# Kernel tuning notes

Measured on AMD Instinct MI355X. Metric: run time of the kernel, lower is better.

## Reference

```python
import jax, jax.numpy as jnp
import numpy as np

B, L, D = 2, 2048, 1024
NUM_HEADS = 16
HEAD_DIM = D // NUM_HEADS


def setup_inputs() -> dict:
    key = jax.random.key(0)
    k1, k2 = jax.random.split(key)
    x = jax.random.normal(k1, (B, L, D), dtype=jnp.float32)
    # torch Linear(input_dim, 3*output_dim, bias=False); store as [in, 3*out] for x @ W
    W_qkv = jax.random.normal(k2, (D, 3 * D), dtype=jnp.float32) * (1.0 / np.sqrt(D))
    return {"x": x, "W_qkv": W_qkv}


def reference(x, W_qkv):
    b, l, d = x.shape
    h, hd = NUM_HEADS, HEAD_DIM
    qkv = x @ W_qkv                                  # [B, L, 3*D]
    qkv = qkv.reshape(b, l, 3, h, hd)
    q = jnp.transpose(qkv[:, :, 0], (0, 2, 1, 3))    # [B, H, L, hd]
    k = jnp.transpose(qkv[:, :, 1], (0, 2, 1, 3))
    v = jnp.transpose(qkv[:, :, 2], (0, 2, 1, 3))
    scale = 1.0 / jnp.sqrt(jnp.asarray(hd, dtype=x.dtype))
    scores = jnp.einsum('bhqd,bhkd->bhqk', q, k) * scale   # [B, H, L, L]
    causal = jnp.triu(jnp.ones((l, l), dtype=bool), k=1)   # True above diagonal -> masked
    scores = jnp.where(causal, -jnp.inf, scores)
    attn = jax.nn.softmax(scores, axis=-1)
    # dropout p=0.0 -> identity (eval mode)
    out = jnp.einsum('bhqk,bhkd->bhqd', attn, v)            # [B, H, L, hd]
    out = jnp.transpose(out, (0, 2, 1, 3)).reshape(b, l, h * hd)
    return out
```

## Files before the change

kernel.cpp:

```cpp
#include <hip/hip_runtime.h>
#include <hip/hip_bf16.h>
#include <math.h>

#define NB_L 2048
#define GM 4096
#define GN 3072
#define GK 1024
#define NROWS 65536
#define SCALE_L2E 0.180336880f

typedef float  f4v __attribute__((ext_vector_type(4)));
typedef short  s4v __attribute__((ext_vector_type(4)));
typedef short  s8v __attribute__((ext_vector_type(8)));

#define MFMA_16x16x32(a, b, c) __builtin_amdgcn_mfma_f32_16x16x32_bf16((a), (b), (c), 0, 0, 0)
#define MFMA_16x16x16(a, b, c) __builtin_amdgcn_mfma_f32_16x16x16bf16_1k((a), (b), (c), 0, 0, 0)

static __device__ __forceinline__ unsigned int bfpk(float a, float b) {
    __hip_bfloat162 h = __float22bfloat162_rn(float2{a, b});
    union { __hip_bfloat162 h2; unsigned int u; } cv; cv.h2 = h; return cv.u;
}
static __device__ __forceinline__ unsigned short bf1(float a) {
    union { __hip_bfloat16 h; unsigned short u; } cv; cv.h = __float2bfloat16(a); return cv.u;
}
static __device__ __forceinline__ float bf2f(unsigned short u) {
    union { unsigned int u; float f; } cv; cv.u = ((unsigned int)u) << 16; return cv.f;
}

static __device__ __forceinline__ void gl_lds16(const ushort* g, ushort* l) {
    __builtin_amdgcn_global_load_lds((const __attribute__((address_space(1))) void*)g,
                                     (__attribute__((address_space(3))) void*)l, 16, 0, 0);
}

__global__ __launch_bounds__(256) void conv_x(const float* __restrict__ X, ushort* __restrict__ Xb) {
    const int i = blockIdx.x * 256 + threadIdx.x;
    const float4 f0 = ((const float4*)X)[2 * i];
    const float4 f1 = ((const float4*)X)[2 * i + 1];
    uint4 u;
    u.x = bfpk(f0.x, f0.y); u.y = bfpk(f0.z, f0.w);
    u.z = bfpk(f1.x, f1.y); u.w = bfpk(f1.z, f1.w);
    ((uint4*)Xb)[i] = u;
}

__global__ __launch_bounds__(256) void conv_wt(const float* __restrict__ W, ushort* __restrict__ Wt) {
    __shared__ __align__(16) ushort T[64][72];
    const int t = threadIdx.x;
    const int k0 = blockIdx.x * 64, n0 = blockIdx.y * 64;
    {
        const int kr = t >> 2, nc0 = (t & 3) * 16;
        const float* src = W + (size_t)(k0 + kr) * GN + n0 + nc0;
#pragma unroll
        for (int u = 0; u < 4; ++u) {
            const float4 v = *(const float4*)(src + 4 * u);
            T[nc0 + 4 * u + 0][kr] = bf1(v.x);
            T[nc0 + 4 * u + 1][kr] = bf1(v.y);
            T[nc0 + 4 * u + 2][kr] = bf1(v.z);
            T[nc0 + 4 * u + 3][kr] = bf1(v.w);
        }
    }
    __syncthreads();
    {
        const int nr = t >> 2, kc0 = (t & 3) * 16;
        ushort* dst = Wt + (size_t)(n0 + nr) * GK + k0 + kc0;
        *(s8v*)dst       = *(const s8v*)&T[nr][kc0];
        *(s8v*)(dst + 8) = *(const s8v*)&T[nr][kc0 + 8];
    }
}

__global__ __launch_bounds__(256) void qkv_gemm_bf16(
    const ushort* __restrict__ Xb, const ushort* __restrict__ Wt,
    ushort* __restrict__ Qh, ushort* __restrict__ Kh, ushort* __restrict__ VT)
{
    __shared__ __align__(16) ushort As[2][4][128][8];
    __shared__ __align__(16) ushort Bs[2][4][128][8];
    const int tid = threadIdx.x;
    const int row0 = blockIdx.y * 128, col0 = blockIdx.x * 128;
    const int mA = tid & 127, k2a = tid >> 7;
    const int lane = tid & 63, w = tid >> 6;
    const int wr = w >> 1, wc = w & 1, lq = lane & 15, quad = lane >> 4;

    f4v acc[4][4];
#pragma unroll
    for (int g = 0; g < 4; ++g)
#pragma unroll
        for (int j = 0; j < 4; ++j) acc[g][j] = 0.f;

    const ushort* gA = Xb + (size_t)(row0 + mA) * GK + k2a * 8;
    const ushort* gB = Wt + (size_t)(col0 + mA) * GK + k2a * 8;

    gl_lds16(gA,      &As[0][k2a][mA][0]);
    gl_lds16(gA + 16, &As[0][k2a + 2][mA][0]);
    gl_lds16(gB,      &Bs[0][k2a][mA][0]);
    gl_lds16(gB + 16, &Bs[0][k2a + 2][mA][0]);

    for (int it = 0; it < 32; ++it) {
        const int cur = it & 1, nxt = cur ^ 1;
        __syncthreads();
        if (it + 1 < 32) {
            const int k0 = (it + 1) * 32;
            gl_lds16(gA + k0,      &As[nxt][k2a][mA][0]);
            gl_lds16(gA + k0 + 16, &As[nxt][k2a + 2][mA][0]);
            gl_lds16(gB + k0,      &Bs[nxt][k2a][mA][0]);
            gl_lds16(gB + k0 + 16, &Bs[nxt][k2a + 2][mA][0]);
        }
        s8v af[4], bfr[4];
#pragma unroll
        for (int g = 0; g < 4; ++g) af[g]  = *(const s8v*)&As[cur][quad][wr * 64 + g * 16 + lq][0];
#pragma unroll
        for (int j = 0; j < 4; ++j) bfr[j] = *(const s8v*)&Bs[cur][quad][wc * 64 + j * 16 + lq][0];
#pragma unroll
        for (int g = 0; g < 4; ++g)
#pragma unroll
            for (int j = 0; j < 4; ++j)
                acc[g][j] = MFMA_16x16x32(af[g], bfr[j], acc[g][j]);
    }

    const int part = blockIdx.x >> 3;
#pragma unroll
    for (int g = 0; g < 4; ++g)
#pragma unroll
        for (int j = 0; j < 4; ++j) {
            const int col = (col0 & 1023) + wc * 64 + j * 16 + lq;
            const int hh = col >> 6, d = col & 63;
#pragma unroll
            for (int r = 0; r < 4; ++r) {
                const int row = row0 + wr * 64 + g * 16 + quad * 4 + r;
                const int b = row >> 11, tok = row & 2047;
                const int bh = b * 16 + hh;
                if (part == 0) {
                    Qh[((size_t)bh * 2048 + tok) * 64 + d] = bf1(acc[g][j][r] * SCALE_L2E);
                } else if (part == 1) {
                    Kh[((size_t)bh * 2048 + tok) * 64 + (d ^ ((tok & 7) << 3))] = bf1(acc[g][j][r]);
                } else {
                    VT[((size_t)bh * 64 + d) * 2048 + (tok ^ ((d & 7) << 3))] = bf1(acc[g][j][r]);
                }
            }
        }
}

__global__ __launch_bounds__(256, 4) void attn_bf16(
    const ushort* __restrict__ Qh, const ushort* __restrict__ Kh,
    const ushort* __restrict__ VT, ushort* __restrict__ Opart, float* __restrict__ Lp)
{
    __shared__ __align__(16) ushort Ks[2][64 * 64];
    __shared__ __align__(16) ushort Vt[2][64 * 64];

    const int x = blockIdx.x;
    const int bh = x & 31;
    const int qlow = (x >> 5) & 7;
    const int s = (x >> 8) & 1;
    const int x9 = (x >> 9) & 1;
    const int qt = x9 ? (15 - qlow) : qlow;

    const int tid = threadIdx.x;
    const int w = tid >> 6, lane = tid & 63;
    const int lq = lane & 15, quad = lane >> 4;
    const int kswz = (lq & 7) << 3;
    const int qrow_base = qt * 128 + w * 32;
    const int diag = 2 * qt + (w >> 1);

    s8v qf[2][2];
#pragma unroll
    for (int qg = 0; qg < 2; ++qg)
#pragma unroll
        for (int sb = 0; sb < 2; ++sb)
            qf[qg][sb] = *(const s8v*)(Qh + ((size_t)bh * 2048 + qrow_base + qg * 16 + lq) * 64
                                       + sb * 32 + quad * 8);

    f4v o[4][2];
#pragma unroll
    for (int dg = 0; dg < 4; ++dg)
#pragma unroll
        for (int qg = 0; qg < 2; ++qg) o[dg][qg] = 0.f;
    f4v lacc[2]; lacc[0] = 0.f; lacc[1] = 0.f;
    const s4v ones = { (short)0x3F80, (short)0x3F80, (short)0x3F80, (short)0x3F80 };

    const int kt_lo = s ? (qt + 1) : 0;
    const int kt_hi = s ? (2 * qt + 1) : qt;
    const int niter = kt_hi - kt_lo + 1;

    const ushort* kbase = Kh + (size_t)bh * 2048 * 64;
    const ushort* vbase = VT + (size_t)bh * 64 * 2048;
    const int g1 = tid, g2 = tid + 256;
    const int kr1 = g1 >> 3, ko1 = (g1 & 7) * 8;
    const int kr2 = g2 >> 3, ko2 = (g2 & 7) * 8;

    auto stage = [&](int kt, int bufi) {
        const ushort* kt_k = kbase + (size_t)kt * 64 * 64;
        const ushort* kt_v = vbase + kt * 64;
        gl_lds16(kt_k + kr1 * 64 + ko1,          &Ks[bufi][g1 * 8]);
        gl_lds16(kt_k + kr2 * 64 + ko2,          &Ks[bufi][g2 * 8]);
        gl_lds16(kt_v + (size_t)kr1 * 2048 + ko1, &Vt[bufi][g1 * 8]);
        gl_lds16(kt_v + (size_t)kr2 * 2048 + ko2, &Vt[bufi][g2 * 8]);
    };

    auto compute = [&](int ktc, int bufi) {
        if (ktc > diag) return;
        f4v st[4][2];
#pragma unroll
        for (int kg = 0; kg < 4; ++kg)
#pragma unroll
            for (int qg = 0; qg < 2; ++qg) st[kg][qg] = 0.f;
#pragma unroll
        for (int kg = 0; kg < 4; ++kg)
#pragma unroll
            for (int sb = 0; sb < 2; ++sb) {
                const s8v af = *(const s8v*)&Ks[bufi][(kg * 16 + lq) * 64
                                                     + ((sb * 32 + quad * 8) ^ kswz)];
#pragma unroll
                for (int qg = 0; qg < 2; ++qg)
                    st[kg][qg] = MFMA_16x16x32(af, qf[qg][sb], st[kg][qg]);
            }
        if (ktc == diag) {
#pragma unroll
            for (int kg = 0; kg < 4; ++kg)
#pragma unroll
                for (int qg = 0; qg < 2; ++qg) {
                    const int qrow = qrow_base + qg * 16 + lq;
#pragma unroll
                    for (int r = 0; r < 4; ++r)
                        if (ktc * 64 + kg * 16 + quad * 4 + r > qrow)
                            st[kg][qg][r] = -INFINITY;
                }
        }
#pragma unroll
        for (int kg = 0; kg < 4; ++kg)
#pragma unroll
            for (int qg = 0; qg < 2; ++qg)
#pragma unroll
                for (int r = 0; r < 4; ++r)
                    st[kg][qg][r] = exp2f(st[kg][qg][r]);
#pragma unroll
        for (int ks = 0; ks < 4; ++ks) {
            s4v pb[2];
#pragma unroll
            for (int qg = 0; qg < 2; ++qg) {
                union { s4v v; uint2 u; } c;
                c.u.x = bfpk(st[ks][qg][0], st[ks][qg][1]);
                c.u.y = bfpk(st[ks][qg][2], st[ks][qg][3]);
                pb[qg] = c.v;
            }
#pragma unroll
            for (int qg = 0; qg < 2; ++qg)
                lacc[qg] = MFMA_16x16x16(ones, pb[qg], lacc[qg]);
#pragma unroll
            for (int dg = 0; dg < 4; ++dg) {
                const s4v va = *(const s4v*)&Vt[bufi][(dg * 16 + lq) * 64
                                                     + ((ks * 16 + quad * 4) ^ kswz)];
#pragma unroll
                for (int qg = 0; qg < 2; ++qg)
                    o[dg][qg] = MFMA_16x16x16(va, pb[qg], o[dg][qg]);
            }
        }
    };

    stage(kt_lo, 0);
    for (int i = 0; i < niter; ++i) {
        const int cur = i & 1;
        __syncthreads();
        if (i + 1 < niter) stage(kt_lo + i + 1, cur ^ 1);
        compute(kt_lo + i, cur);
    }

#pragma unroll
    for (int qg = 0; qg < 2; ++qg) {
        const size_t prow = (size_t)(s * 32 + bh) * 2048 + qrow_base + qg * 16 + lq;
#pragma unroll
        for (int dg = 0; dg < 4; ++dg) {
            const int d = dg * 16 + quad * 4;
            uint2 u;
            u.x = bfpk(o[dg][qg][0], o[dg][qg][1]);
            u.y = bfpk(o[dg][qg][2], o[dg][qg][3]);
            *(uint2*)&Opart[prow * 64 + d] = u;
        }
        if (quad == 0) Lp[prow] = lacc[qg][0];
    }
}

__global__ __launch_bounds__(256) void attn_combine(
    const ushort* __restrict__ Opart, const float* __restrict__ Lp, float* __restrict__ Out)
{
    const int id = blockIdx.x * 256 + threadIdx.x;
    const int row = id >> 4, c4 = (id & 15) * 4;
    const float l0 = Lp[row], l1 = Lp[row + NROWS];
    const float inv = 1.0f / (l0 + l1);

    const s4v a = *(const s4v*)&Opart[(size_t)row * 64 + c4];
    const s4v c = *(const s4v*)&Opart[(size_t)(row + NROWS) * 64 + c4];
    float4 v;
    v.x = (bf2f((unsigned short)a[0]) + bf2f((unsigned short)c[0])) * inv;
    v.y = (bf2f((unsigned short)a[1]) + bf2f((unsigned short)c[1])) * inv;
    v.z = (bf2f((unsigned short)a[2]) + bf2f((unsigned short)c[2])) * inv;
    v.w = (bf2f((unsigned short)a[3]) + bf2f((unsigned short)c[3])) * inv;

    const int bh = row >> 11, qrow = row & 2047;
    const int b = bh >> 4, h = bh & 15;
    *(float4*)(Out + ((size_t)(b * 2048 + qrow)) * 1024 + h * 64 + c4) = v;
}

extern "C" void kernel_launch(void* const* d_in, const int* in_sizes, int n_in,
                              void* d_out, int out_size, void* d_ws, size_t ws_size,
                              hipStream_t stream)
{
    const float* x  = (const float*)d_in[0];
    const float* wq = (const float*)d_in[1];
    float* out = (float*)d_out;

    const size_t HEADTEN = (size_t)32 * 2048 * 64;
    ushort* wsp = (ushort*)d_ws;
    ushort* qh = wsp;
    ushort* kh = qh + HEADTEN;
    ushort* vt = kh + HEADTEN;
    ushort* xb = vt + HEADTEN;
    ushort* wt = xb + (size_t)GM * GK;
    ushort* opart = xb;
    float*  lp    = (float*)(opart + (size_t)2 * NROWS * 64);

    conv_x<<<GM * GK / (256 * 8), 256, 0, stream>>>(x, xb);
    conv_wt<<<dim3(GK / 64, GN / 64), 256, 0, stream>>>(wq, wt);
    qkv_gemm_bf16<<<dim3(GN / 128, GM / 128), 256, 0, stream>>>(xb, wt, qh, kh, vt);
    attn_bf16<<<1024, 256, 0, stream>>>(qh, kh, vt, opart, lp);
    attn_combine<<<NROWS * 16 / 256, 256, 0, stream>>>(opart, lp, out);
}
```

Before: 189.6 us.

## Fuse bf16 conversion kernels and retile QKV GEMM to 128x96 blocks

After: 202.6 us. 6.9% more time.

```diff
diff --git a/kernel.cpp b/kernel.cpp
--- a/kernel.cpp
+++ b/kernel.cpp
@@ -32,96 +32,110 @@
                                      (__attribute__((address_space(3))) void*)l, 16, 0, 0);
 }
 
-__global__ __launch_bounds__(256) void conv_x(const float* __restrict__ X, ushort* __restrict__ Xb) {
-    const int i = blockIdx.x * 256 + threadIdx.x;
-    const float4 f0 = ((const float4*)X)[2 * i];
-    const float4 f1 = ((const float4*)X)[2 * i + 1];
-    uint4 u;
-    u.x = bfpk(f0.x, f0.y); u.y = bfpk(f0.z, f0.w);
-    u.z = bfpk(f1.x, f1.y); u.w = bfpk(f1.z, f1.w);
-    ((uint4*)Xb)[i] = u;
-}
-
-__global__ __launch_bounds__(256) void conv_wt(const float* __restrict__ W, ushort* __restrict__ Wt) {
+__global__ __launch_bounds__(256) void conv_fused(
+    const float* __restrict__ X, const float* __restrict__ W,
+    ushort* __restrict__ Xb, ushort* __restrict__ Wt)
+{
     __shared__ __align__(16) ushort T[64][72];
-    const int t = threadIdx.x;
-    const int k0 = blockIdx.x * 64, n0 = blockIdx.y * 64;
-    {
-        const int kr = t >> 2, nc0 = (t & 3) * 16;
-        const float* src = W + (size_t)(k0 + kr) * GN + n0 + nc0;
-#pragma unroll
-        for (int u = 0; u < 4; ++u) {
-            const float4 v = *(const float4*)(src + 4 * u);
-            T[nc0 + 4 * u + 0][kr] = bf1(v.x);
-            T[nc0 + 4 * u + 1][kr] = bf1(v.y);
-            T[nc0 + 4 * u + 2][kr] = bf1(v.z);
-            T[nc0 + 4 * u + 3][kr] = bf1(v.w);
-        }
-    }
-    __syncthreads();
-    {
-        const int nr = t >> 2, kc0 = (t & 3) * 16;
-        ushort* dst = Wt + (size_t)(n0 + nr) * GK + k0 + kc0;
-        *(s8v*)dst       = *(const s8v*)&T[nr][kc0];
-        *(s8v*)(dst + 8) = *(const s8v*)&T[nr][kc0 + 8];
-    }
-}
-
-__global__ __launch_bounds__(256) void qkv_gemm_bf16(
+    const int bid = blockIdx.x, t = threadIdx.x;
+    if (bid < 2048) {
+        const int i = bid * 256 + t;
+        const float4 f0 = ((const float4*)X)[2 * i];
+        const float4 f1 = ((const float4*)X)[2 * i + 1];
+        uint4 u;
+        u.x = bfpk(f0.x, f0.y); u.y = bfpk(f0.z, f0.w);
+        u.z = bfpk(f1.x, f1.y); u.w = bfpk(f1.z, f1.w);
+        ((uint4*)Xb)[i] = u;
+    } else {
+        const int wb = bid - 2048;
+        const int k0 = (wb & 15) * 64, n0 = (wb >> 4) * 64;
+        {
+            const int kr = t >> 2, nc0 = (t & 3) * 16;
+            const float* src = W + (size_t)(k0 + kr) * GN + n0 + nc0;
+#pragma unroll
+            for (int u = 0; u < 4; ++u) {
+                const float4 v = *(const float4*)(src + 4 * u);
+                T[nc0 + 4 * u + 0][kr] = bf1(v.x);
+                T[nc0 + 4 * u + 1][kr] = bf1(v.y);
+                T[nc0 + 4 * u + 2][kr] = bf1(v.z);
+                T[nc0 + 4 * u + 3][kr] = bf1(v.w);
+            }
+        }
+        __syncthreads();
+        {
+            const int nr = t >> 2, kc0 = (t & 3) * 16;
+            ushort* dst = Wt + (size_t)(n0 + nr) * GK + k0 + kc0;
+            *(s8v*)dst       = *(const s8v*)&T[nr][kc0];
+            *(s8v*)(dst + 8) = *(const s8v*)&T[nr][kc0 + 8];
+        }
+    }
+}
+
+__global__ __launch_bounds__(256, 4) void qkv_gemm_bf16(
     const ushort* __restrict__ Xb, const ushort* __restrict__ Wt,
     ushort* __restrict__ Qh, ushort* __restrict__ Kh, ushort* __restrict__ VT)
 {
-    __shared__ __align__(16) ushort As[2][4][128][8];
-    __shared__ __align__(16) ushort Bs[2][4][128][8];
+    __shared__ __align__(16) ushort As[2][4 * 128 * 8];
+    __shared__ __align__(16) ushort Bs[2][4 * 128 * 8];
     const int tid = threadIdx.x;
-    const int row0 = blockIdx.y * 128, col0 = blockIdx.x * 128;
-    const int mA = tid & 127, k2a = tid >> 7;
+    const int row0 = blockIdx.y * 128, col0 = blockIdx.x * 96;
     const int lane = tid & 63, w = tid >> 6;
     const int wr = w >> 1, wc = w & 1, lq = lane & 15, quad = lane >> 4;
 
-    f4v acc[4][4];
+    f4v acc[4][3];
 #pragma unroll
     for (int g = 0; g < 4; ++g)
 #pragma unroll
-        for (int j = 0; j < 4; ++j) acc[g][j] = 0.f;
-
-    const ushort* gA = Xb + (size_t)(row0 + mA) * GK + k2a * 8;
-    const ushort* gB = Wt + (size_t)(col0 + mA) * GK + k2a * 8;
-
-    gl_lds16(gA,      &As[0][k2a][mA][0]);
-    gl_lds16(gA + 16, &As[0][k2a + 2][mA][0]);
-    gl_lds16(gB,      &Bs[0][k2a][mA][0]);
-    gl_lds16(gB + 16, &Bs[0][k2a + 2][mA][0]);
+        for (int j = 0; j < 3; ++j) acc[g][j] = 0.f;
+
+    const int sr = tid & 127;
+    const bool bok = sr < 96;
+    const ushort* gA1 = Xb + (size_t)(row0 + sr) * GK + (tid >> 7) * 8;
+    const ushort* gA2 = gA1 + 16;
+    const ushort* gB1 = Wt + (size_t)(col0 + sr) * GK + (tid >> 7) * 8;
+    const ushort* gB2 = gB1 + 16;
+    const int d1 = tid * 8, d2 = (tid + 256) * 8;
+
+    gl_lds16(gA1, &As[0][d1]);
+    gl_lds16(gA2, &As[0][d2]);
+    if (bok) {
+        gl_lds16(gB1, &Bs[0][d1]);
+        gl_lds16(gB2, &Bs[0][d2]);
+    }
 
     for (int it = 0; it < 32; ++it) {
         const int cur = it & 1, nxt = cur ^ 1;
         __syncthreads();
         if (it + 1 < 32) {
             const int k0 = (it + 1) * 32;
-            gl_lds16(gA + k0,      &As[nxt][k2a][mA][0]);
-            gl_lds16(gA + k0 + 16, &As[nxt][k2a + 2][mA][0]);
-            gl_lds16(gB + k0,      &Bs[nxt][k2a][mA][0]);
-            gl_lds16(gB + k0 + 16, &Bs[nxt][k2a + 2][mA][0]);
-        }
-        s8v af[4], bfr[4];
-#pragma unroll
-        for (int g = 0; g < 4; ++g) af[g]  = *(const s8v*)&As[cur][quad][wr * 64 + g * 16 + lq][0];
-#pragma unroll
-        for (int j = 0; j < 4; ++j) bfr[j] = *(const s8v*)&Bs[cur][quad][wc * 64 + j * 16 + lq][0];
+            gl_lds16(gA1 + k0, &As[nxt][d1]);
+            gl_lds16(gA2 + k0, &As[nxt][d2]);
+            if (bok) {
+                gl_lds16(gB1 + k0, &Bs[nxt][d1]);
+                gl_lds16(gB2 + k0, &Bs[nxt][d2]);
+            }
+        }
+        s8v af[4], bfr[3];
 #pragma unroll
         for (int g = 0; g < 4; ++g)
-#pragma unroll
-            for (int j = 0; j < 4; ++j)
+            af[g]  = *(const s8v*)&As[cur][(quad * 128 + wr * 64 + g * 16 + lq) * 8];
+#pragma unroll
+        for (int j = 0; j < 3; ++j)
+            bfr[j] = *(const s8v*)&Bs[cur][(quad * 128 + wc * 48 + j * 16 + lq) * 8];
+#pragma unroll
+        for (int g = 0; g < 4; ++g)
+#pragma unroll
+            for (int j = 0; j < 3; ++j)
                 acc[g][j] = MFMA_16x16x32(af[g], bfr[j], acc[g][j]);
     }
 
-    const int part = blockIdx.x >> 3;
 #pragma unroll
     for (int g = 0; g < 4; ++g)
 #pragma unroll
-        for (int j = 0; j < 4; ++j) {
-            const int col = (col0 & 1023) + wc * 64 + j * 16 + lq;
-            const int hh = col >> 6, d = col & 63;
+        for (int j = 0; j < 3; ++j) {
+            const int col = col0 + wc * 48 + j * 16 + lq;
+            const int part = col >> 10, colp = col & 1023;
+            const int hh = colp >> 6, d = colp & 63;
 #pragma unroll
             for (int r = 0; r < 4; ++r) {
                 const int row = row0 + wr * 64 + g * 16 + quad * 4 + r;
@@ -188,8 +202,8 @@
     auto stage = [&](int kt, int bufi) {
         const ushort* kt_k = kbase + (size_t)kt * 64 * 64;
         const ushort* kt_v = vbase + kt * 64;
-        gl_lds16(kt_k + kr1 * 64 + ko1,          &Ks[bufi][g1 * 8]);
-        gl_lds16(kt_k + kr2 * 64 + ko2,          &Ks[bufi][g2 * 8]);
+        gl_lds16(kt_k + kr1 * 64 + ko1,           &Ks[bufi][g1 * 8]);
+        gl_lds16(kt_k + kr2 * 64 + ko2,           &Ks[bufi][g2 * 8]);
         gl_lds16(kt_v + (size_t)kr1 * 2048 + ko1, &Vt[bufi][g1 * 8]);
         gl_lds16(kt_v + (size_t)kr2 * 2048 + ko2, &Vt[bufi][g2 * 8]);
     };
@@ -316,9 +330,8 @@
     ushort* opart = xb;
     float*  lp    = (float*)(opart + (size_t)2 * NROWS * 64);
 
-    conv_x<<<GM * GK / (256 * 8), 256, 0, stream>>>(x, xb);
-    conv_wt<<<dim3(GK / 64, GN / 64), 256, 0, stream>>>(wq, wt);
-    qkv_gemm_bf16<<<dim3(GN / 128, GM / 128), 256, 0, stream>>>(xb, wt, qh, kh, vt);
+    conv_fused<<<2816, 256, 0, stream>>>(x, wq, xb, wt);
+    qkv_gemm_bf16<<<dim3(32, 32), 256, 0, stream>>>(xb, wt, qh, kh, vt);
     attn_bf16<<<1024, 256, 0, stream>>>(qh, kh, vt, opart, lp);
     attn_combine<<<NROWS * 16 / 256, 256, 0, stream>>>(opart, lp, out);
 }
```
